# Kernel tuning notes

Measured on AMD Instinct MI355X. Metric: run time of the kernel, lower is better.

Reference implementation:

```python
import jax, jax.numpy as jnp
import numpy as np


def setup_inputs() -> dict:
    key = jax.random.key(0)
    k1, k2 = jax.random.split(key)
    z = jax.random.normal(k1, (16, 256, 64, 64), dtype=jnp.float32)
    # codebook initialized uniform(-1/size, 1/size) in the original; values don't
    # affect the math path, use same distribution for realism
    size, code_dim = 1024, 256
    weight = jax.random.uniform(k2, (size, code_dim), dtype=jnp.float32,
                                minval=-1.0 / size, maxval=1.0 / size)
    return {"z": z, "weight": weight}


def reference(z, weight):
    b, c, h, w = z.shape  # c == code_dim
    flat = jnp.transpose(z, (0, 2, 3, 1)).reshape(-1, c)  # [N, D]
    # squared L2 distances via ||a-b||^2 = ||a||^2 - 2 a.b + ||b||^2
    d = (jnp.sum(flat * flat, axis=1, keepdims=True)
         - 2.0 * flat @ weight.T
         + jnp.sum(weight * weight, axis=1))  # [N, size]
    encoding_indices = jnp.argmin(d, axis=-1).reshape(b, h, w)  # int indices
    quantized = jnp.transpose(weight[encoding_indices], (0, 3, 1, 2))  # [b,c,h,w]
    straight_through = jax.lax.stop_gradient(quantized - z) + z
    return quantized, straight_through, encoding_indices
```

## Files before the change

kernel.cpp:

```cpp
#include <hip/hip_runtime.h>


#define NROWS 65536
#define DDIM 256
#define KCODES 1024
#define TAU 2e-4f
#define WWIN 2e-4f

typedef unsigned long long u64;
typedef _Float16 f16x8 __attribute__((ext_vector_type(8)));
typedef float f32x4 __attribute__((ext_vector_type(4)));

__device__ __forceinline__ void gld16(const void* g, void* l) {
    __builtin_amdgcn_global_load_lds((const __attribute__((address_space(1))) void*)g,
                                     (__attribute__((address_space(3))) void*)l, 16, 0, 0);
}

template <typename F>
__device__ __forceinline__ float np_pairwise256_sq(F get) {
    float half[2];
#pragma unroll
    for (int h = 0; h < 2; ++h) {
        float r[8];
#pragma unroll
        for (int j = 0; j < 8; ++j) { float v = get(h * 128 + j); r[j] = __fmul_rn(v, v); }
        for (int i = 8; i < 128; i += 8)
#pragma unroll
            for (int j = 0; j < 8; ++j) {
                float v = get(h * 128 + i + j);
                r[j] = __fadd_rn(r[j], __fmul_rn(v, v));
            }
        half[h] = __fadd_rn(__fadd_rn(__fadd_rn(r[0], r[1]), __fadd_rn(r[2], r[3])),
                            __fadd_rn(__fadd_rn(r[4], r[5]), __fadd_rn(r[6], r[7])));
    }
    return __fadd_rn(half[0], half[1]);
}

__global__ void prep_w_k(const float* __restrict__ w, f16x8* __restrict__ w16,
                         float* __restrict__ wn) {
    int bid = blockIdx.x;
    if (bid < 128) {
        int idx = bid * 256 + threadIdx.x;
        int o = idx >> 10, c = idx & 1023;
        const float* wp = w + (size_t)c * DDIM + o * 8;
        f16x8 hv;
#pragma unroll
        for (int j = 0; j < 8; ++j) hv[j] = (_Float16)(wp[j] * 1024.0f);
        w16[(size_t)o * 1024 + c] = hv;
    } else {
        int k = (bid - 128) * 256 + threadIdx.x;
        const float* wp = w + (size_t)k * DDIM;
        wn[k] = np_pairwise256_sq([&](int i) { return wp[i]; });
    }
}

#define DPP_MIN(CTRL) {                                                                 \
    float ov = __int_as_float(__builtin_amdgcn_mov_dpp(__float_as_int(bv), CTRL, 0xf, 0xf, false)); \
    bv = fminf(bv, ov); }

__device__ __forceinline__ int aswz(int row) {
    return (row * 16) ^ (((row >> 2) & 7) << 4);
}

__launch_bounds__(512, 2)
__global__ void argmin_fused_k(const float* __restrict__ z, const f16x8* __restrict__ w16,
                               const float* __restrict__ wn,
                               float* __restrict__ btv, u64* __restrict__ bmk) {
    __shared__ char arena[81920];
    char* lA = arena;
    char* lB = arena + 65536;
    const int t = threadIdx.x;
    const int lane = t & 63;
    const int l15 = lane & 15, l4 = lane >> 4;
    const int wid = t >> 6;
    const int wm = wid >> 1;
    const int wn_ = wid & 1;
    const int p = blockIdx.x;
    const int n0 = (((p & 7) << 6) | (p >> 3)) << 7;
    const float* zb = z + (size_t)(n0 >> 12) * 1048576 + (n0 & 4095);

    auto STAGE_B = [&](int cb, int s, int buf) {
        int o = s * 4 + (wid >> 1);
        int half = wid & 1;
        gld16(w16 + (size_t)(o * 1024 + cb * 128 + half * 64 + lane),
              lB + buf * 8192 + wid * 1024);
    };
    STAGE_B(0, 0, 0);

    {
        int oc = t >> 5;
        int rq = t & 31;
#pragma unroll
        for (int p2 = 0; p2 < 2; ++p2) {
            int o = p2 * 16 + oc;
            float4 L[8];
#pragma unroll
            for (int j = 0; j < 8; ++j)
                L[j] = *reinterpret_cast<const float4*>(zb + (size_t)(o * 8 + j) * 4096 + rq * 4);
#pragma unroll
            for (int k = 0; k < 4; ++k) {
                f16x8 rec;
#pragma unroll
                for (int j = 0; j < 8; ++j) {
                    const float* lj = reinterpret_cast<const float*>(&L[j]);
                    rec[j] = (_Float16)lj[k];
                }
                *reinterpret_cast<f16x8*>(lA + o * 2048 + aswz(rq * 4 + k)) = rec;
            }
        }
    }
    __syncthreads();

    auto COMPUTE = [&](int s, int buf, f32x4 (&acc)[2][4]) {
        f16x8 a[2], b[4];
        const char* pb = lB + buf * 8192 + l4 * 2048 + (wn_ * 64 + l15) * 16;
#pragma unroll
        for (int nt = 0; nt < 4; ++nt) b[nt] = *reinterpret_cast<const f16x8*>(pb + nt * 256);
        const char* pa = lA + (s * 4 + l4) * 2048;
#pragma unroll
        for (int mt = 0; mt < 2; ++mt)
            a[mt] = *reinterpret_cast<const f16x8*>(pa + aswz(wm * 32 + mt * 16 + l15));
#pragma unroll
        for (int mt = 0; mt < 2; ++mt)
#pragma unroll
            for (int nt = 0; nt < 4; ++nt)
                acc[mt][nt] = __builtin_amdgcn_mfma_f32_16x16x32_f16(a[mt], b[nt], acc[mt][nt], 0, 0, 0);
    };

#pragma unroll 1
    for (int cb = 0; cb < 8; ++cb) {
        f32x4 acc[2][4];
#pragma unroll
        for (int mt = 0; mt < 2; ++mt)
#pragma unroll
            for (int nt = 0; nt < 4; ++nt) acc[mt][nt] = f32x4{0.f, 0.f, 0.f, 0.f};

#pragma unroll
        for (int s = 0; s < 8; ++s) {
            if (s < 7)       STAGE_B(cb, s + 1, (s + 1) & 1);
            else if (cb < 7) STAGE_B(cb + 1, 0, 0);
            if (s == 7 && cb == 7) { asm volatile("s_waitcnt vmcnt(0)" ::: "memory"); }
            else                   { asm volatile("s_waitcnt vmcnt(1)" ::: "memory"); }
            __builtin_amdgcn_s_barrier();
            COMPUTE(s, s & 1, acc);
            __builtin_amdgcn_s_barrier();
        }

        const int c0 = cb << 7;
        float wnv[4];
#pragma unroll
        for (int nt = 0; nt < 4; ++nt) wnv[nt] = wn[c0 + wn_ * 64 + nt * 16 + l15];
        const int ebase = ((cb << 1) | wn_) << 16;
#pragma unroll
        for (int mt = 0; mt < 2; ++mt) {
#pragma unroll
            for (int r = 0; r < 4; ++r) {
                float s0 = fmaf(-0.001953125f, acc[mt][0][r], wnv[0]);
                float s1 = fmaf(-0.001953125f, acc[mt][1][r], wnv[1]);
                float s2 = fmaf(-0.001953125f, acc[mt][2][r], wnv[2]);
                float s3 = fmaf(-0.001953125f, acc[mt][3][r], wnv[3]);
                float bv = fminf(fminf(s0, s1), fminf(s2, s3));
                DPP_MIN(0xB1)
                DPP_MIN(0x4E)
                DPP_MIN(0x141)
                DPP_MIN(0x140)
                float thr = bv + WWIN;
                u64 b0 = __ballot(s0 < thr), b1 = __ballot(s1 < thr);
                u64 b2 = __ballot(s2 < thr), b3 = __ballot(s3 < thr);
                int sh = 16 * l4;
                u64 msk = ((b0 >> sh) & 0xFFFFull)
                        | (((b1 >> sh) & 0xFFFFull) << 16)
                        | (((b2 >> sh) & 0xFFFFull) << 32)
                        | (((b3 >> sh) & 0xFFFFull) << 48);
                if (l15 == 0) {
                    int row = wm * 32 + mt * 16 + l4 * 4 + r;
                    btv[ebase + n0 + row] = bv;
                    bmk[ebase + n0 + row] = msk;
                }
            }
        }
    }
}

__launch_bounds__(256, 2)
__global__ void finrescue_k(const float* __restrict__ z, const float* __restrict__ w,
                            const float* __restrict__ s2,
                            const float* __restrict__ btv, const u64* __restrict__ bmk,
                            float* __restrict__ idxf_out) {
    __shared__ float zsh[4][16][260];
    const int t = threadIdx.x;
    const int lane = t & 63;
    const int wid = t >> 6;
    const int p = blockIdx.x;
    const int grp = (((p & 7) << 7) | (p >> 3)) * 4 + wid;
    const int n0 = grp * 16;
    const int r = lane >> 2;
    const int eq = lane & 3;
    const int n = n0 + r;

    float v0 = btv[((eq * 4 + 0) << 16) + n];
    float v1 = btv[((eq * 4 + 1) << 16) + n];
    float v2 = btv[((eq * 4 + 2) << 16) + n];
    float v3 = btv[((eq * 4 + 3) << 16) + n];
    float bv = 3.4e38f, b2 = 3.4e38f;
    int be = 0;
    {
        if (v0 < bv) { b2 = bv; bv = v0; be = eq * 4 + 0; } else b2 = fminf(b2, v0);
        if (v1 < bv) { b2 = bv; bv = v1; be = eq * 4 + 1; } else b2 = fminf(b2, v1);
        if (v2 < bv) { b2 = bv; bv = v2; be = eq * 4 + 2; } else b2 = fminf(b2, v2);
        if (v3 < bv) { b2 = bv; bv = v3; be = eq * 4 + 3; } else b2 = fminf(b2, v3);
    }
#pragma unroll
    for (int m = 1; m < 4; m <<= 1) {
        float ov = __shfl_xor(bv, m), o2 = __shfl_xor(b2, m);
        int oe = __shfl_xor(be, m);
        if (ov < bv || (ov == bv && oe < be)) { b2 = fminf(bv, o2); bv = ov; be = oe; }
        else b2 = fminf(b2, ov);
    }
    u64 wmask = bmk[((u64)be << 16) + n];
    int bi = be * 64 + (int)(__ffsll((long long)wmask) - 1);
    bool flag = (__popcll(wmask) > 1) || (b2 - bv < TAU);
    if (eq == 0) idxf_out[n] = (float)bi;

    u64 bal0 = __ballot(v0 <= bv + TAU);
    u64 bal1 = __ballot(v1 <= bv + TAU);
    u64 bal2 = __ballot(v2 <= bv + TAU);
    u64 bal3 = __ballot(v3 <= bv + TAU);

    u64 fb = __ballot(flag);
    if ((fb & 0x1111111111111111ull) == 0) return;

    const float* zb = z + (size_t)(n0 >> 12) * 1048576 + (n0 & 4095);
#pragma unroll
    for (int it = 0; it < 16; ++it) {
        int d = it * 16 + (lane >> 2);
        float4 v = *reinterpret_cast<const float4*>(zb + (size_t)d * 4096 + (lane & 3) * 4);
        zsh[wid][(lane & 3) * 4 + 0][d] = v.x;
        zsh[wid][(lane & 3) * 4 + 1][d] = v.y;
        zsh[wid][(lane & 3) * 4 + 2][d] = v.z;
        zsh[wid][(lane & 3) * 4 + 3][d] = v.w;
    }
    asm volatile("s_waitcnt lgkmcnt(0)" ::: "memory");
    __builtin_amdgcn_sched_barrier(0);

#pragma unroll 1
    for (int r2 = 0; r2 < 16; ++r2) {
        if (!((fb >> (r2 * 4)) & 1)) continue;
        int nn = n0 + r2;
        int hh = (lane >> 3) & 1, jj = lane & 7;
        float w0 = zsh[wid][r2][hh * 128 + jj];
        float accj = __fmul_rn(w0, w0);
#pragma unroll
        for (int i = 1; i < 16; ++i) {
            float w2 = zsh[wid][r2][hh * 128 + i * 8 + jj];
            accj = __fadd_rn(accj, __fmul_rn(w2, w2));
        }
        float a1 = __fadd_rn(accj, __shfl_xor(accj, 1));
        float a2 = __fadd_rn(a1, __shfl_xor(a1, 2));
        float a4 = __fadd_rn(a2, __shfl_xor(a2, 4));
        float s1 = __fadd_rn(a4, __shfl_xor(a4, 8));

        float4 zr4 = *reinterpret_cast<const float4*>(&zsh[wid][r2][lane * 4]);
        float bv2 = 3.4e38f;
        int   bi2 = 0;
#pragma unroll
        for (int e = 0; e < 16; ++e) {
            u64 bal = (e & 3) == 0 ? bal0 : (e & 3) == 1 ? bal1 : (e & 3) == 2 ? bal2 : bal3;
            if ((bal >> (r2 * 4 + (e >> 2))) & 1) {
                u64 m = bmk[((u64)e << 16) + nn];
                while (m) {
                    int k = __ffsll((long long)m) - 1;
                    m &= m - 1;
                    int c = e * 64 + k;
                    const float* wp = w + (size_t)c * DDIM + lane * 4;
                    double md = 0.0;
                    md = fma((double)zr4.x, (double)wp[0], md);
                    md = fma((double)zr4.y, (double)wp[1], md);
                    md = fma((double)zr4.z, (double)wp[2], md);
                    md = fma((double)zr4.w, (double)wp[3], md);
#pragma unroll
                    for (int mm = 1; mm < 64; mm <<= 1) md += __shfl_xor(md, mm);
                    float dq = __fadd_rn((float)((double)s1 - 2.0 * md), s2[c]);
                    if (dq < bv2) { bv2 = dq; bi2 = c; }
                }
            }
        }
        if (lane == 0) idxf_out[nn] = (float)bi2;
    }
}

__global__ void gather_k(const float* __restrict__ idxf, const float* __restrict__ w,
                         float* __restrict__ out0, float* __restrict__ out1) {
    int tid = blockIdx.x * 256 + threadIdx.x;
    int n   = tid & 65535;
    int c4  = tid >> 16;
    int code = (int)idxf[n];
    float4 v = *reinterpret_cast<const float4*>(w + (size_t)code * DDIM + c4 * 4);
    size_t off = (size_t)(n >> 12) * 1048576 + (size_t)c4 * 4 * 4096 + (n & 4095);
    out0[off]         = v.x;
    out0[off + 4096]  = v.y;
    out0[off + 8192]  = v.z;
    out0[off + 12288] = v.w;
    out1[off]         = v.x;
    out1[off + 4096]  = v.y;
    out1[off + 8192]  = v.z;
    out1[off + 12288] = v.w;
}

extern "C" void kernel_launch(void* const* d_in, const int* in_sizes, int n_in,
                              void* d_out, int out_size, void* d_ws, size_t ws_size,
                              hipStream_t stream) {
    const float* z = (const float*)d_in[0];
    const float* w = (const float*)d_in[1];
    float* out    = (float*)d_out;
    float* out0   = out;
    float* out1   = out + 16777216;
    float* outidx = out + 33554432;

    char* s1b = (char*)out1;
    f16x8* w16 = (f16x8*)s1b;
    float* wn  = (float*)(s1b + 1048576);
    float* btv = (float*)(s1b + 2097152);
    u64*   bmk = (u64*)(s1b + 10485760);

    prep_w_k<<<132, 256, 0, stream>>>(w, w16, wn);
    argmin_fused_k<<<NROWS / 128, 512, 0, stream>>>(z, w16, wn, btv, bmk);
    finrescue_k<<<NROWS / 64, 256, 0, stream>>>(z, w, wn, btv, bmk, outidx);
    gather_k<<<NROWS * 64 / 256, 256, 0, stream>>>(outidx, w, out0, out1);
}
```

Baseline: 103.7 us.

## Fuse codebook gather into rescue kernel and use workspace for scratch

Adds a templated rescue body. When enough workspace is available, it writes the final code index to shared memory and then gathers the codebook rows straight into both outputs. This removes the separate gather launch and its re-read of the index buffer. The scratch buffers move from the second output region into the provided workspace, so the outputs can be written in the same kernel without overwriting scratch data. The fused stores cover only 16 contiguous rows per channel, which may coalesce worse than the original gather.

```diff
diff --git a/kernel.cpp b/kernel.cpp
--- a/kernel.cpp
+++ b/kernel.cpp
@@ -182,12 +182,13 @@
     }
 }
 
-__launch_bounds__(256, 2)
-__global__ void finrescue_k(const float* __restrict__ z, const float* __restrict__ w,
-                            const float* __restrict__ s2,
-                            const float* __restrict__ btv, const u64* __restrict__ bmk,
-                            float* __restrict__ idxf_out) {
-    __shared__ float zsh[4][16][260];
+template <bool FUSE_GATHER>
+__device__ __forceinline__ void finrescue_body(
+        const float* __restrict__ z, const float* __restrict__ w,
+        const float* __restrict__ s2, const float* __restrict__ btv,
+        const u64* __restrict__ bmk, float* __restrict__ idxf_out,
+        float* __restrict__ out0, float* __restrict__ out1,
+        float (*zsh)[16][260], int (*codes)[16]) {
     const int t = threadIdx.x;
     const int lane = t & 63;
     const int wid = t >> 6;
@@ -220,7 +221,10 @@
     u64 wmask = bmk[((u64)be << 16) + n];
     int bi = be * 64 + (int)(__ffsll((long long)wmask) - 1);
     bool flag = (__popcll(wmask) > 1) || (b2 - bv < TAU);
-    if (eq == 0) idxf_out[n] = (float)bi;
+    if (eq == 0) {
+        idxf_out[n] = (float)bi;
+        if (FUSE_GATHER) codes[wid][r] = bi;
+    }
 
     u64 bal0 = __ballot(v0 <= bv + TAU);
     u64 bal1 = __ballot(v1 <= bv + TAU);
@@ -228,65 +232,109 @@
     u64 bal3 = __ballot(v3 <= bv + TAU);
 
     u64 fb = __ballot(flag);
-    if ((fb & 0x1111111111111111ull) == 0) return;
-
-    const float* zb = z + (size_t)(n0 >> 12) * 1048576 + (n0 & 4095);
-#pragma unroll
-    for (int it = 0; it < 16; ++it) {
-        int d = it * 16 + (lane >> 2);
-        float4 v = *reinterpret_cast<const float4*>(zb + (size_t)d * 4096 + (lane & 3) * 4);
-        zsh[wid][(lane & 3) * 4 + 0][d] = v.x;
-        zsh[wid][(lane & 3) * 4 + 1][d] = v.y;
-        zsh[wid][(lane & 3) * 4 + 2][d] = v.z;
-        zsh[wid][(lane & 3) * 4 + 3][d] = v.w;
-    }
-    asm volatile("s_waitcnt lgkmcnt(0)" ::: "memory");
-    __builtin_amdgcn_sched_barrier(0);
+    if ((fb & 0x1111111111111111ull) != 0) {
+        const float* zb = z + (size_t)(n0 >> 12) * 1048576 + (n0 & 4095);
+#pragma unroll
+        for (int it = 0; it < 16; ++it) {
+            int d = it * 16 + (lane >> 2);
+            float4 v = *reinterpret_cast<const float4*>(zb + (size_t)d * 4096 + (lane & 3) * 4);
+            zsh[wid][(lane & 3) * 4 + 0][d] = v.x;
+            zsh[wid][(lane & 3) * 4 + 1][d] = v.y;
+            zsh[wid][(lane & 3) * 4 + 2][d] = v.z;
+            zsh[wid][(lane & 3) * 4 + 3][d] = v.w;
+        }
+        asm volatile("s_waitcnt lgkmcnt(0)" ::: "memory");
+        __builtin_amdgcn_sched_barrier(0);
 
 #pragma unroll 1
-    for (int r2 = 0; r2 < 16; ++r2) {
-        if (!((fb >> (r2 * 4)) & 1)) continue;
-        int nn = n0 + r2;
-        int hh = (lane >> 3) & 1, jj = lane & 7;
-        float w0 = zsh[wid][r2][hh * 128 + jj];
-        float accj = __fmul_rn(w0, w0);
-#pragma unroll
-        for (int i = 1; i < 16; ++i) {
-            float w2 = zsh[wid][r2][hh * 128 + i * 8 + jj];
-            accj = __fadd_rn(accj, __fmul_rn(w2, w2));
-        }
-        float a1 = __fadd_rn(accj, __shfl_xor(accj, 1));
-        float a2 = __fadd_rn(a1, __shfl_xor(a1, 2));
-        float a4 = __fadd_rn(a2, __shfl_xor(a2, 4));
-        float s1 = __fadd_rn(a4, __shfl_xor(a4, 8));
-
-        float4 zr4 = *reinterpret_cast<const float4*>(&zsh[wid][r2][lane * 4]);
-        float bv2 = 3.4e38f;
-        int   bi2 = 0;
-#pragma unroll
-        for (int e = 0; e < 16; ++e) {
-            u64 bal = (e & 3) == 0 ? bal0 : (e & 3) == 1 ? bal1 : (e & 3) == 2 ? bal2 : bal3;
-            if ((bal >> (r2 * 4 + (e >> 2))) & 1) {
-                u64 m = bmk[((u64)e << 16) + nn];
-                while (m) {
-                    int k = __ffsll((long long)m) - 1;
-                    m &= m - 1;
-                    int c = e * 64 + k;
-                    const float* wp = w + (size_t)c * DDIM + lane * 4;
-                    double md = 0.0;
-                    md = fma((double)zr4.x, (double)wp[0], md);
-                    md = fma((double)zr4.y, (double)wp[1], md);
-                    md = fma((double)zr4.z, (double)wp[2], md);
-                    md = fma((double)zr4.w, (double)wp[3], md);
-#pragma unroll
-                    for (int mm = 1; mm < 64; mm <<= 1) md += __shfl_xor(md, mm);
-                    float dq = __fadd_rn((float)((double)s1 - 2.0 * md), s2[c]);
-                    if (dq < bv2) { bv2 = dq; bi2 = c; }
+        for (int r2 = 0; r2 < 16; ++r2) {
+            if (!((fb >> (r2 * 4)) & 1)) continue;
+            int nn = n0 + r2;
+            int hh = (lane >> 3) & 1, jj = lane & 7;
+            float w0 = zsh[wid][r2][hh * 128 + jj];
+            float accj = __fmul_rn(w0, w0);
+#pragma unroll
+            for (int i = 1; i < 16; ++i) {
+                float w2 = zsh[wid][r2][hh * 128 + i * 8 + jj];
+                accj = __fadd_rn(accj, __fmul_rn(w2, w2));
+            }
+            float a1 = __fadd_rn(accj, __shfl_xor(accj, 1));
+            float a2 = __fadd_rn(a1, __shfl_xor(a1, 2));
+            float a4 = __fadd_rn(a2, __shfl_xor(a2, 4));
+            float s1 = __fadd_rn(a4, __shfl_xor(a4, 8));
+
+            float4 zr4 = *reinterpret_cast<const float4*>(&zsh[wid][r2][lane * 4]);
+            float bv2 = 3.4e38f;
+            int   bi2 = 0;
+#pragma unroll
+            for (int e = 0; e < 16; ++e) {
+                u64 bal = (e & 3) == 0 ? bal0 : (e & 3) == 1 ? bal1 : (e & 3) == 2 ? bal2 : bal3;
+                if ((bal >> (r2 * 4 + (e >> 2))) & 1) {
+                    u64 m = bmk[((u64)e << 16) + nn];
+                    while (m) {
+                        int k = __ffsll((long long)m) - 1;
+                        m &= m - 1;
+                        int c = e * 64 + k;
+                        const float* wp = w + (size_t)c * DDIM + lane * 4;
+                        double md = 0.0;
+                        md = fma((double)zr4.x, (double)wp[0], md);
+                        md = fma((double)zr4.y, (double)wp[1], md);
+                        md = fma((double)zr4.z, (double)wp[2], md);
+                        md = fma((double)zr4.w, (double)wp[3], md);
+#pragma unroll
+                        for (int mm = 1; mm < 64; mm <<= 1) md += __shfl_xor(md, mm);
+                        float dq = __fadd_rn((float)((double)s1 - 2.0 * md), s2[c]);
+                        if (dq < bv2) { bv2 = dq; bi2 = c; }
+                    }
                 }
             }
-        }
-        if (lane == 0) idxf_out[nn] = (float)bi2;
-    }
+            if (lane == 0) {
+                idxf_out[nn] = (float)bi2;
+                if (FUSE_GATHER) codes[wid][r2] = bi2;
+            }
+        }
+    }
+
+    if (FUSE_GATHER) {
+        asm volatile("s_waitcnt lgkmcnt(0)" ::: "memory");
+        __builtin_amdgcn_sched_barrier(0);
+        int nr = lane & 15, c4 = lane >> 4;
+        int code = codes[wid][nr];
+        int nn = n0 + nr;
+        size_t base = (size_t)(nn >> 12) * 1048576 + (nn & 4095);
+#pragma unroll 4
+        for (int p2 = 0; p2 < 16; ++p2) {
+            int c = p2 * 16 + c4 * 4;
+            float4 v = *reinterpret_cast<const float4*>(w + (size_t)code * DDIM + c);
+            size_t o = base + (size_t)c * 4096;
+            out0[o]         = v.x;
+            out0[o + 4096]  = v.y;
+            out0[o + 8192]  = v.z;
+            out0[o + 12288] = v.w;
+            out1[o]         = v.x;
+            out1[o + 4096]  = v.y;
+            out1[o + 8192]  = v.z;
+            out1[o + 12288] = v.w;
+        }
+    }
+}
+
+__launch_bounds__(256, 2)
+__global__ void finrescue_gather_k(const float* __restrict__ z, const float* __restrict__ w,
+                                   const float* __restrict__ s2, const float* __restrict__ btv,
+                                   const u64* __restrict__ bmk, float* __restrict__ idxf_out,
+                                   float* __restrict__ out0, float* __restrict__ out1) {
+    __shared__ float zsh[4][16][260];
+    __shared__ int codes[4][16];
+    finrescue_body<true>(z, w, s2, btv, bmk, idxf_out, out0, out1, zsh, codes);
+}
+
+__launch_bounds__(256, 2)
+__global__ void finrescue_k(const float* __restrict__ z, const float* __restrict__ w,
+                            const float* __restrict__ s2, const float* __restrict__ btv,
+                            const u64* __restrict__ bmk, float* __restrict__ idxf_out) {
+    __shared__ float zsh[4][16][260];
+    finrescue_body<false>(z, w, s2, btv, bmk, idxf_out, nullptr, nullptr, zsh, nullptr);
 }
 
 __global__ void gather_k(const float* __restrict__ idxf, const float* __restrict__ w,
@@ -317,14 +365,27 @@
     float* out1   = out + 16777216;
     float* outidx = out + 33554432;
 
-    char* s1b = (char*)out1;
-    f16x8* w16 = (f16x8*)s1b;
-    float* wn  = (float*)(s1b + 1048576);
-    float* btv = (float*)(s1b + 2097152);
-    u64*   bmk = (u64*)(s1b + 10485760);
-
-    prep_w_k<<<132, 256, 0, stream>>>(w, w16, wn);
-    argmin_fused_k<<<NROWS / 128, 512, 0, stream>>>(z, w16, wn, btv, bmk);
-    finrescue_k<<<NROWS / 64, 256, 0, stream>>>(z, w, wn, btv, bmk, outidx);
-    gather_k<<<NROWS * 64 / 256, 256, 0, stream>>>(outidx, w, out0, out1);
-}
+    if (ws_size >= (size_t)14 * 1024 * 1024) {
+        char* sb = (char*)d_ws;
+        f16x8* w16 = (f16x8*)sb;
+        float* wn  = (float*)(sb + 1048576);
+        float* btv = (float*)(sb + 2097152);
+        u64*   bmk = (u64*)(sb + 6291456);
+
+        prep_w_k<<<132, 256, 0, stream>>>(w, w16, wn);
+        argmin_fused_k<<<NROWS / 128, 512, 0, stream>>>(z, w16, wn, btv, bmk);
+        finrescue_gather_k<<<NROWS / 64, 256, 0, stream>>>(z, w, wn, btv, bmk,
+                                                           outidx, out0, out1);
+    } else {
+        char* s1b = (char*)out1;
+        f16x8* w16 = (f16x8*)s1b;
+        float* wn  = (float*)(s1b + 1048576);
+        float* btv = (float*)(s1b + 2097152);
+        u64*   bmk = (u64*)(s1b + 10485760);
+
+        prep_w_k<<<132, 256, 0, stream>>>(w, w16, wn);
+        argmin_fused_k<<<NROWS / 128, 512, 0, stream>>>(z, w16, wn, btv, bmk);
+        finrescue_k<<<NROWS / 64, 256, 0, stream>>>(z, w, wn, btv, bmk, outidx);
+        gather_k<<<NROWS * 64 / 256, 256, 0, stream>>>(outidx, w, out0, out1);
+    }
+}
```

New measurement: 99.55 us (median of 2 runs). 4.0% less time.
